# Performance work log

Hardware: AMD Instinct MI355X
Metric: run time of the kernel (lower is better)

## Reference

```python
import jax, jax.numpy as jnp
import numpy as np

N, D, K, A, BINS, DEPTH = 1024, 384, 64, 5, 64, 4
D_MAX = 22.0


def _expected_distance(distogram):
    # distance_one_hot_inverse(softmax(distogram), 0.0, 22.0, 64)
    step = D_MAX / BINS
    centers = step * jnp.arange(BINS, dtype=distogram.dtype) + step / 2
    p = jax.nn.softmax(distogram, axis=-1)  # [N,N,BINS]
    return (p * centers).sum(axis=-1)       # [N,N]


def _extract_neighbours(pos, prev_pos, distogram, resi, chain, batch, mask, key):
    inf = jnp.inf
    same_batch = batch[:, None] == batch[None, :]
    same_chain = (chain[:, None] == chain[None, :]) & same_batch
    pair_mask = mask[:, None] & mask[None, :] & same_batch
    # sequence-separation distance (only within a chain), 3.81 A per residue
    seq_d = jnp.where(same_chain,
                      jnp.abs(resi[:, None] - resi[None, :]).astype(jnp.float32) * 3.81,
                      inf)
    md = _expected_distance(distogram)
    d = jnp.minimum(seq_d, jnp.where(md < 8.0, md, inf))
    ca = pos[:, 1]                                   # current CA positions [N,3]
    d = jnp.minimum(d, jnp.linalg.norm(ca[:, None] - ca[None, :], axis=-1))
    pca = prev_pos[:, 1]
    d = jnp.minimum(d, jnp.linalg.norm(pca[:, None] - pca[None, :], axis=-1))
    d = jnp.where(same_batch, d, inf)
    log_p = -3.0 * d
    u = jax.random.uniform(key, d.shape)
    gumbel = -jnp.log(-jnp.log(u + 1e-6) + 1e-6)
    random_distance = -(log_p + gumbel)
    random_distance = jnp.where(pair_mask, random_distance, inf)
    neg_vals, idx = jax.lax.top_k(-random_distance, K)  # k smallest random distances
    nbr_mask = jnp.isfinite(neg_vals)                   # invalid neighbours have -inf
    return idx, nbr_mask                                # [N,K] int32, [N,K] bool


def setup_inputs() -> dict:
    key = jax.random.key(0)
    ks = jax.random.split(key, 8)
    local = jax.random.normal(ks[0], (N, D), dtype=jnp.float32)
    pos = 3.0 * jax.random.normal(ks[1], (N, A, 3), dtype=jnp.float32)
    prev_pos = 3.0 * jax.random.normal(ks[2], (N, A, 3), dtype=jnp.float32)
    distogram = jax.random.normal(ks[3], (N, N, BINS), dtype=jnp.float32)
    Wn = jax.random.normal(ks[4], (D, D), dtype=jnp.float32) / np.sqrt(D)
    Wp = 0.01 * jax.random.normal(ks[5], (D, A * 3), dtype=jnp.float32)
    ar = jnp.arange(N, dtype=jnp.int32)
    batch = ar // 256          # 4 proteins of 256 residues
    chain = (ar // 128) % 2    # 2 chains per protein
    resi = ar % 128            # residue index within chain
    mask = jnp.ones((N,), dtype=bool)
    return {"local": local, "pos": pos, "prev_pos": prev_pos, "distogram": distogram,
            "Wn": Wn, "Wp": Wp, "resi": resi, "chain": chain, "batch": batch, "mask": mask}


def reference(local, pos, prev_pos, distogram, Wn, Wp, resi, chain, batch, mask):
    mask_f = mask.astype(local.dtype)
    key = jax.random.key(42)
    traj = []
    for t in range(DEPTH):  # diffusion_depth iterations, neighbours recomputed each block
        idx, nbr_mask = _extract_neighbours(pos, prev_pos, distogram, resi, chain,
                                            batch, mask, jax.random.fold_in(key, t))
        nf = local[idx] * nbr_mask[..., None].astype(local.dtype)   # [N,K,D]
        cnt = jnp.maximum(nbr_mask.sum(axis=1, keepdims=True).astype(local.dtype), 1.0)
        msg = nf.sum(axis=1) / cnt                                   # [N,D]
        local = local + jax.nn.gelu(msg @ Wn)
        pos = pos + 0.1 * (local @ Wp).reshape(N, A, 3) * mask_f[:, None, None]
        traj.append(pos)
    trajectory = jnp.stack(traj)  # [DEPTH,N,A,3]
    return local, pos, trajectory
```

## Files before the change

kernel.cpp:

```cpp
#include <hip/hip_runtime.h>
#include <stdint.h>

typedef unsigned int u32;
typedef unsigned long long u64;

#define NN 1024
#define DDIM 384
#define KNB 64
#define BINS_ 64
#define DEPTH_ 4

#define OUT_POS 393216
#define OUT_TRAJ 408576

__device__ __forceinline__ u32 rotl32(u32 x, int r) { return (x << r) | (x >> (32 - r)); }

__device__ __forceinline__ void threefry(u32 k0, u32 k1, u32 x0, u32 x1, u32& o0, u32& o1) {
  u32 ks2 = k0 ^ k1 ^ 0x1BD11BDAu;
#define TF_R(r) { x0 += x1; x1 = rotl32(x1, r); x1 ^= x0; }
  x0 += k0; x1 += k1;
  TF_R(13) TF_R(15) TF_R(26) TF_R(6)
  x0 += k1; x1 += ks2 + 1u;
  TF_R(17) TF_R(29) TF_R(16) TF_R(24)
  x0 += ks2; x1 += k0 + 2u;
  TF_R(13) TF_R(15) TF_R(26) TF_R(6)
  x0 += k0; x1 += k1 + 3u;
  TF_R(17) TF_R(29) TF_R(16) TF_R(24)
  x0 += k1; x1 += ks2 + 4u;
  TF_R(13) TF_R(15) TF_R(26) TF_R(6)
  x0 += ks2; x1 += k0 + 5u;
#undef TF_R
  o0 = x0; o1 = x1;
}

__global__ void k_init(const float* __restrict__ lin, const float* __restrict__ pin,
                       float* __restrict__ localf, float* __restrict__ posf) {
  int id = blockIdx.x * 256 + threadIdx.x;
  if (id < NN * DDIM) localf[id] = lin[id];
  else posf[id - NN * DDIM] = pin[id - NN * DDIM];
}

__global__ __launch_bounds__(256) void k_dstatic(
    const float* __restrict__ disto, const float* __restrict__ ppos,
    const int* __restrict__ resi, const int* __restrict__ chain,
    const int* __restrict__ batch, float* __restrict__ dstat) {
  int p = blockIdx.x * 256 + threadIdx.x;
  int i = p >> 10, j = p & 1023;
  if (batch[i] != batch[j]) { dstat[p] = __builtin_inff(); return; }
  float seq_d = __builtin_inff();
  if (chain[i] == chain[j]) {
    int dr = resi[i] - resi[j];
    seq_d = __fmul_rn(fabsf((float)dr), 3.81f);
  }
  const float4* dp = reinterpret_cast<const float4*>(disto + (size_t)p * BINS_);
  float w[BINS_];
#pragma unroll
  for (int q = 0; q < 16; ++q) {
    float4 v = dp[q];
    w[4*q+0] = v.x; w[4*q+1] = v.y; w[4*q+2] = v.z; w[4*q+3] = v.w;
  }
  float m = -__builtin_inff();
#pragma unroll
  for (int q = 0; q < BINS_; ++q) m = fmaxf(m, w[q]);
  float s = 0.f;
#pragma unroll
  for (int q = 0; q < BINS_; ++q) {
    w[q] = expf(__fsub_rn(w[q], m));
    s = __fadd_rn(s, w[q]);
  }
  float e = 0.f;
#pragma unroll
  for (int q = 0; q < BINS_; ++q) {
    float pq = __fdiv_rn(w[q], s);
    e = __fadd_rn(e, __fmul_rn(pq, 0.34375f * (float)q + 0.171875f));
  }
  float md = e;
  float d = fminf(seq_d, (md < 8.0f) ? md : __builtin_inff());
  float ax = __fsub_rn(ppos[i*15+3], ppos[j*15+3]);
  float ay = __fsub_rn(ppos[i*15+4], ppos[j*15+4]);
  float az = __fsub_rn(ppos[i*15+5], ppos[j*15+5]);
  float ss = __fadd_rn(__fadd_rn(__fmul_rn(ax,ax), __fmul_rn(ay,ay)), __fmul_rn(az,az));
  dstat[p] = fminf(d, __fsqrt_rn(ss));
}

__global__ __launch_bounds__(256) void k_topk(
    const float* __restrict__ dstat, const float* __restrict__ posf,
    const int* __restrict__ batch,
    int t, int* __restrict__ idx, float* __restrict__ cntv) {
  int i = blockIdx.x;
  __shared__ u32 skm[NN];
  __shared__ int sjj[NN];
  int bi = batch[i];
  float cax = posf[i*15+3], cay = posf[i*15+4], caz = posf[i*15+5];
  u32 fk0, fk1;
  threefry(0u, 42u, 0u, (u32)t, fk0, fk1);
  for (int j = threadIdx.x; j < NN; j += 256) {
    float rd = __builtin_inff();
    if (batch[j] == bi) {
      float d = dstat[i*NN + j];
      float dx = __fsub_rn(cax, posf[j*15+3]);
      float dy = __fsub_rn(cay, posf[j*15+4]);
      float dz = __fsub_rn(caz, posf[j*15+5]);
      float ss = __fadd_rn(__fadd_rn(__fmul_rn(dx,dx), __fmul_rn(dy,dy)), __fmul_rn(dz,dz));
      d = fminf(d, __fsqrt_rn(ss));
      u32 o0, o1;
      threefry(fk0, fk1, 0u, (u32)(i*NN + j), o0, o1);
      u32 bits = o0 ^ o1;
      float u = __fsub_rn(__uint_as_float((bits >> 9) | 0x3f800000u), 1.0f);
      float inner = __fadd_rn(-logf(__fadd_rn(u, 1e-6f)), 1e-6f);
      float gum = -logf(inner);
      float logp = __fmul_rn(-3.0f, d);
      rd = -__fadd_rn(logp, gum);
    }
    u32 fb = __float_as_uint(rd);
    u32 km = (fb & 0x80000000u) ? ~fb : (fb | 0x80000000u);
    skm[j] = km; sjj[j] = j;
  }
  for (int size = 2; size <= NN; size <<= 1) {
    for (int stride = size >> 1; stride > 0; stride >>= 1) {
      __syncthreads();
      for (int tt = threadIdx.x; tt < NN/2; tt += 256) {
        int a = ((tt & ~(stride-1)) << 1) | (tt & (stride-1));
        int b = a | stride;
        u32 ka = skm[a], kb = skm[b];
        int ja = sjj[a], jb = sjj[b];
        bool gt = (ka > kb) || ((ka == kb) && (ja > jb));
        bool asc = ((a & size) == 0);
        if (gt == asc) { skm[a] = kb; skm[b] = ka; sjj[a] = jb; sjj[b] = ja; }
      }
    }
  }
  __syncthreads();
  if (threadIdx.x < KNB) {
    u32 km = skm[threadIdx.x];
    bool fin = (km < 0xFF800000u);
    idx[i*KNB + threadIdx.x] = fin ? sjj[threadIdx.x] : -1;
    u64 ball = __ballot(fin);
    if (threadIdx.x == 0) cntv[i] = fmaxf((float)__popcll(ball), 1.0f);
  }
}

__global__ __launch_bounds__(384) void k_msg(
    const float* __restrict__ localf, const int* __restrict__ idx,
    const float* __restrict__ cntv, const float* __restrict__ Wn,
    float* __restrict__ g) {
  int i = blockIdx.x; int d = threadIdx.x;
  __shared__ int sidx[KNB];
  __shared__ float msgL[DDIM];
  if (d < KNB) sidx[d] = idx[i*KNB + d];
  __syncthreads();
  float s = 0.f;
#pragma unroll 8
  for (int k = 0; k < KNB; ++k) {
    int id = sidx[k];
    if (id >= 0) s += localf[id*DDIM + d];
  }
  msgL[d] = s / cntv[i];
  __syncthreads();
  float acc = 0.f;
#pragma unroll 8
  for (int dd = 0; dd < DDIM; ++dd) acc = fmaf(msgL[dd], Wn[dd*DDIM + d], acc);
  float x = acc;
  float th = tanhf(0.7978845608028654f * (x + 0.044715f * x * x * x));
  g[i*DDIM + d] = 0.5f * x * (1.0f + th);
}

__global__ __launch_bounds__(64) void k_update(
    float* __restrict__ localf, const float* __restrict__ g,
    const float* __restrict__ Wp,
    float* __restrict__ posf, float* __restrict__ out, int t) {
  int i = blockIdx.x;
  __shared__ float lr[DDIM];
  for (int d = threadIdx.x; d < DDIM; d += 64) {
    float v = localf[i*DDIM + d] + g[i*DDIM + d];
    localf[i*DDIM + d] = v;
    lr[d] = v;
  }
  __syncthreads();
  if (threadIdx.x < 15) {
    int c = threadIdx.x;
    float acc = 0.f;
#pragma unroll 8
    for (int d = 0; d < DDIM; ++d) acc = fmaf(lr[d], Wp[d*15 + c], acc);
    float pv = posf[i*15 + c] + 0.1f * acc;
    posf[i*15 + c] = pv;
    out[OUT_TRAJ + t*15360 + i*15 + c] = pv;
  }
}

__global__ void k_out(const float* __restrict__ localf, const float* __restrict__ posf,
                      float* __restrict__ out) {
  int id = blockIdx.x * 256 + threadIdx.x;
  if (id < NN * DDIM) out[id] = localf[id];
  else out[id] = posf[id - NN * DDIM];
}

extern "C" void kernel_launch(void* const* d_in, const int* in_sizes, int n_in,
                              void* d_out, int out_size, void* d_ws, size_t ws_size,
                              hipStream_t stream) {
  (void)in_sizes; (void)n_in; (void)out_size; (void)ws_size;
  const float* local_in = (const float*)d_in[0];
  const float* pos_in   = (const float*)d_in[1];
  const float* ppos_in  = (const float*)d_in[2];
  const float* disto    = (const float*)d_in[3];
  const float* Wn       = (const float*)d_in[4];
  const float* Wp       = (const float*)d_in[5];
  const int* resi       = (const int*)d_in[6];
  const int* chain      = (const int*)d_in[7];
  const int* batch      = (const int*)d_in[8];
  float* out = (float*)d_out;
  char* ws = (char*)d_ws;
  float* localf = (float*)(ws + 0);
  float* posf   = (float*)(ws + 1572864);
  float* g      = (float*)(ws + 1634304);
  float* dstat  = (float*)(ws + 3207168);
  int*   idx    = (int*)(ws + 7401472);
  float* cntv   = (float*)(ws + 7663616);

  k_init<<<dim3(1596), dim3(256), 0, stream>>>(local_in, pos_in, localf, posf);
  k_dstatic<<<dim3(4096), dim3(256), 0, stream>>>(disto, ppos_in, resi, chain, batch, dstat);
  for (int t = 0; t < DEPTH_; ++t) {
    k_topk<<<dim3(NN), dim3(256), 0, stream>>>(dstat, posf, batch, t, idx, cntv);
    k_msg<<<dim3(NN), dim3(DDIM), 0, stream>>>(localf, idx, cntv, Wn, g);
    k_update<<<dim3(NN), dim3(64), 0, stream>>>(localf, g, Wp, posf, out, t);
  }
  k_out<<<dim3(1596), dim3(256), 0, stream>>>(localf, posf, out);
}
```

Measured before the change: 661.7 us.

## Fuse top-k, message, and update into one per-round kernel with wave-level sort

Replaces the three per-round kernels with a single k_round kernel that handles four rows per block. Each wave builds 64-bit key/index pairs in registers and selects the top-64 through shuffle-based bitonic sorts and merges, replacing the 1024-element shared-memory bitonic sort with its many __syncthreads. It shares each Wn load across four rows, ping-pongs the local/pos buffers so the init and output copy kernels can go away, and writes the final round straight to the output. The fused kernel launches only 256 blocks, so the GPU may be less fully occupied, and register pressure from the 16 u64 values per lane could cause spills.

```diff
diff --git a/kernel.cpp b/kernel.cpp
--- a/kernel.cpp
+++ b/kernel.cpp
@@ -33,11 +33,23 @@
   o0 = x0; o1 = x1;
 }
 
-__global__ void k_init(const float* __restrict__ lin, const float* __restrict__ pin,
-                       float* __restrict__ localf, float* __restrict__ posf) {
-  int id = blockIdx.x * 256 + threadIdx.x;
-  if (id < NN * DDIM) localf[id] = lin[id];
-  else posf[id - NN * DDIM] = pin[id - NN * DDIM];
+static inline u32 h_rotl32(u32 x, int r) { return (x << r) | (x >> (32 - r)); }
+static void h_threefry(u32 k0, u32 k1, u32 x0, u32 x1, u32& o0, u32& o1) {
+  u32 ks2 = k0 ^ k1 ^ 0x1BD11BDAu;
+#define TF_R(r) { x0 += x1; x1 = h_rotl32(x1, r); x1 ^= x0; }
+  x0 += k0; x1 += k1;
+  TF_R(13) TF_R(15) TF_R(26) TF_R(6)
+  x0 += k1; x1 += ks2 + 1u;
+  TF_R(17) TF_R(29) TF_R(16) TF_R(24)
+  x0 += ks2; x1 += k0 + 2u;
+  TF_R(13) TF_R(15) TF_R(26) TF_R(6)
+  x0 += k0; x1 += k1 + 3u;
+  TF_R(17) TF_R(29) TF_R(16) TF_R(24)
+  x0 += k1; x1 += ks2 + 4u;
+  TF_R(13) TF_R(15) TF_R(26) TF_R(6)
+  x0 += ks2; x1 += k0 + 5u;
+#undef TF_R
+  o0 = x0; o1 = x1;
 }
 
 __global__ __launch_bounds__(256) void k_dstatic(
@@ -83,116 +95,143 @@
   dstat[p] = fminf(d, __fsqrt_rn(ss));
 }
 
-__global__ __launch_bounds__(256) void k_topk(
-    const float* __restrict__ dstat, const float* __restrict__ posf,
-    const int* __restrict__ batch,
-    int t, int* __restrict__ idx, float* __restrict__ cntv) {
-  int i = blockIdx.x;
-  __shared__ u32 skm[NN];
-  __shared__ int sjj[NN];
-  int bi = batch[i];
-  float cax = posf[i*15+3], cay = posf[i*15+4], caz = posf[i*15+5];
-  u32 fk0, fk1;
-  threefry(0u, 42u, 0u, (u32)t, fk0, fk1);
-  for (int j = threadIdx.x; j < NN; j += 256) {
-    float rd = __builtin_inff();
-    if (batch[j] == bi) {
-      float d = dstat[i*NN + j];
-      float dx = __fsub_rn(cax, posf[j*15+3]);
-      float dy = __fsub_rn(cay, posf[j*15+4]);
-      float dz = __fsub_rn(caz, posf[j*15+5]);
-      float ss = __fadd_rn(__fadd_rn(__fmul_rn(dx,dx), __fmul_rn(dy,dy)), __fmul_rn(dz,dz));
-      d = fminf(d, __fsqrt_rn(ss));
-      u32 o0, o1;
-      threefry(fk0, fk1, 0u, (u32)(i*NN + j), o0, o1);
-      u32 bits = o0 ^ o1;
-      float u = __fsub_rn(__uint_as_float((bits >> 9) | 0x3f800000u), 1.0f);
-      float inner = __fadd_rn(-logf(__fadd_rn(u, 1e-6f)), 1e-6f);
-      float gum = -logf(inner);
-      float logp = __fmul_rn(-3.0f, d);
-      rd = -__fadd_rn(logp, gum);
-    }
-    u32 fb = __float_as_uint(rd);
-    u32 km = (fb & 0x80000000u) ? ~fb : (fb | 0x80000000u);
-    skm[j] = km; sjj[j] = j;
-  }
-  for (int size = 2; size <= NN; size <<= 1) {
-    for (int stride = size >> 1; stride > 0; stride >>= 1) {
-      __syncthreads();
-      for (int tt = threadIdx.x; tt < NN/2; tt += 256) {
-        int a = ((tt & ~(stride-1)) << 1) | (tt & (stride-1));
-        int b = a | stride;
-        u32 ka = skm[a], kb = skm[b];
-        int ja = sjj[a], jb = sjj[b];
-        bool gt = (ka > kb) || ((ka == kb) && (ja > jb));
-        bool asc = ((a & size) == 0);
-        if (gt == asc) { skm[a] = kb; skm[b] = ka; sjj[a] = jb; sjj[b] = ja; }
+__device__ __forceinline__ u64 shx64(u64 x, int m) {
+  int lo = __shfl_xor((int)(u32)x, m, 64);
+  int hi = __shfl_xor((int)(u32)(x >> 32), m, 64);
+  return ((u64)(u32)hi << 32) | (u32)lo;
+}
+
+__device__ __forceinline__ u64 merge64(u64 a, u64 b, int lane) {
+  u64 br = shx64(b, 63);
+  u64 m = (a < br) ? a : br;
+  for (int stride = 32; stride > 0; stride >>= 1) {
+    u64 p = shx64(m, stride);
+    u64 lo = (m < p) ? m : p;
+    u64 hi = (m < p) ? p : m;
+    m = ((lane & stride) == 0) ? lo : hi;
+  }
+  return m;
+}
+
+__global__ __launch_bounds__(384) void k_round(
+    const float* __restrict__ dstat, const float* __restrict__ Lprev,
+    float* __restrict__ Lnext, const float* __restrict__ posP,
+    float* __restrict__ posN, const int* __restrict__ batch,
+    const float* __restrict__ Wn, const float* __restrict__ Wp,
+    float* __restrict__ out, int t, u32 fk0, u32 fk1) {
+  __shared__ int sidx[4][KNB];
+  __shared__ float cntL[4];
+  __shared__ float msgT[4][DDIM];
+  __shared__ float lrT[4][DDIM + 1];
+  const int tid = threadIdx.x;
+  const int w = tid >> 6, lane = tid & 63;
+  const int i0 = blockIdx.x * 4;
+
+  if (w < 4) {
+    const int i = i0 + w;
+    const int bi = batch[i];
+    const float cax = posP[i*15+3], cay = posP[i*15+4], caz = posP[i*15+5];
+    u64 v[16];
+#pragma unroll
+    for (int c = 0; c < 16; ++c) {
+      int j = c*64 + lane;
+      float rd = __builtin_inff();
+      if (batch[j] == bi) {
+        float d = dstat[i*NN + j];
+        float dx = __fsub_rn(cax, posP[j*15+3]);
+        float dy = __fsub_rn(cay, posP[j*15+4]);
+        float dz = __fsub_rn(caz, posP[j*15+5]);
+        float ss = __fadd_rn(__fadd_rn(__fmul_rn(dx,dx), __fmul_rn(dy,dy)), __fmul_rn(dz,dz));
+        d = fminf(d, __fsqrt_rn(ss));
+        u32 o0, o1;
+        threefry(fk0, fk1, 0u, (u32)(i*NN + j), o0, o1);
+        u32 bits = o0 ^ o1;
+        float u = __fsub_rn(__uint_as_float((bits >> 9) | 0x3f800000u), 1.0f);
+        float inner = __fadd_rn(-logf(__fadd_rn(u, 1e-6f)), 1e-6f);
+        float gum = -logf(inner);
+        float logp = __fmul_rn(-3.0f, d);
+        rd = -__fadd_rn(logp, gum);
       }
-    }
+      u32 fb = __float_as_uint(rd);
+      u32 km = (fb & 0x80000000u) ? ~fb : (fb | 0x80000000u);
+      v[c] = ((u64)km << 32) | (u32)j;
+    }
+    for (int size = 2; size <= 64; size <<= 1) {
+      for (int stride = size >> 1; stride > 0; stride >>= 1) {
+        bool keepmin = (((lane & stride) == 0) == ((lane & size) == 0));
+#pragma unroll
+        for (int c = 0; c < 16; ++c) {
+          u64 p = shx64(v[c], stride);
+          u64 lo = (v[c] < p) ? v[c] : p;
+          u64 hi = (v[c] < p) ? p : v[c];
+          v[c] = keepmin ? lo : hi;
+        }
+      }
+    }
+#pragma unroll
+    for (int c = 0; c < 8; ++c) v[c] = merge64(v[2*c], v[2*c+1], lane);
+#pragma unroll
+    for (int c = 0; c < 4; ++c) v[c] = merge64(v[2*c], v[2*c+1], lane);
+#pragma unroll
+    for (int c = 0; c < 2; ++c) v[c] = merge64(v[2*c], v[2*c+1], lane);
+    u64 m = merge64(v[0], v[1], lane);
+    u32 km = (u32)(m >> 32);
+    bool fin = (km < 0xFF800000u);
+    sidx[w][lane] = fin ? (int)(u32)(m & 0xffffffffu) : -1;
+    u64 ball = __ballot(fin);
+    if (lane == 0) cntL[w] = fmaxf((float)__popcll(ball), 1.0f);
   }
   __syncthreads();
-  if (threadIdx.x < KNB) {
-    u32 km = skm[threadIdx.x];
-    bool fin = (km < 0xFF800000u);
-    idx[i*KNB + threadIdx.x] = fin ? sjj[threadIdx.x] : -1;
-    u64 ball = __ballot(fin);
-    if (threadIdx.x == 0) cntv[i] = fmaxf((float)__popcll(ball), 1.0f);
-  }
-}
-
-__global__ __launch_bounds__(384) void k_msg(
-    const float* __restrict__ localf, const int* __restrict__ idx,
-    const float* __restrict__ cntv, const float* __restrict__ Wn,
-    float* __restrict__ g) {
-  int i = blockIdx.x; int d = threadIdx.x;
-  __shared__ int sidx[KNB];
-  __shared__ float msgL[DDIM];
-  if (d < KNB) sidx[d] = idx[i*KNB + d];
+
+  {
+    const int c = tid;
+#pragma unroll
+    for (int r = 0; r < 4; ++r) {
+      float s = 0.f;
+#pragma unroll 8
+      for (int k = 0; k < KNB; ++k) {
+        int id = sidx[r][k];
+        if (id >= 0) s += Lprev[id*DDIM + c];
+      }
+      msgT[r][c] = s / cntL[r];
+    }
+  }
   __syncthreads();
-  float s = 0.f;
+
+  {
+    const int c = tid;
+    float a0 = 0.f, a1 = 0.f, a2 = 0.f, a3 = 0.f;
 #pragma unroll 8
-  for (int k = 0; k < KNB; ++k) {
-    int id = sidx[k];
-    if (id >= 0) s += localf[id*DDIM + d];
-  }
-  msgL[d] = s / cntv[i];
+    for (int dd = 0; dd < DDIM; ++dd) {
+      float wv = Wn[dd*DDIM + c];
+      a0 = fmaf(msgT[0][dd], wv, a0);
+      a1 = fmaf(msgT[1][dd], wv, a1);
+      a2 = fmaf(msgT[2][dd], wv, a2);
+      a3 = fmaf(msgT[3][dd], wv, a3);
+    }
+    float accs[4] = {a0, a1, a2, a3};
+#pragma unroll
+    for (int r = 0; r < 4; ++r) {
+      float x = accs[r];
+      float th = tanhf(0.7978845608028654f * (x + 0.044715f * x * x * x));
+      float g = 0.5f * x * (1.0f + th);
+      float ln = Lprev[(i0 + r)*DDIM + c] + g;
+      Lnext[(i0 + r)*DDIM + c] = ln;
+      lrT[r][c] = ln;
+    }
+  }
   __syncthreads();
-  float acc = 0.f;
-#pragma unroll 8
-  for (int dd = 0; dd < DDIM; ++dd) acc = fmaf(msgL[dd], Wn[dd*DDIM + d], acc);
-  float x = acc;
-  float th = tanhf(0.7978845608028654f * (x + 0.044715f * x * x * x));
-  g[i*DDIM + d] = 0.5f * x * (1.0f + th);
-}
-
-__global__ __launch_bounds__(64) void k_update(
-    float* __restrict__ localf, const float* __restrict__ g,
-    const float* __restrict__ Wp,
-    float* __restrict__ posf, float* __restrict__ out, int t) {
-  int i = blockIdx.x;
-  __shared__ float lr[DDIM];
-  for (int d = threadIdx.x; d < DDIM; d += 64) {
-    float v = localf[i*DDIM + d] + g[i*DDIM + d];
-    localf[i*DDIM + d] = v;
-    lr[d] = v;
-  }
-  __syncthreads();
-  if (threadIdx.x < 15) {
-    int c = threadIdx.x;
+
+  if (tid < 60) {
+    const int r = tid / 15, cc = tid % 15;
+    const int i = i0 + r;
     float acc = 0.f;
 #pragma unroll 8
-    for (int d = 0; d < DDIM; ++d) acc = fmaf(lr[d], Wp[d*15 + c], acc);
-    float pv = posf[i*15 + c] + 0.1f * acc;
-    posf[i*15 + c] = pv;
-    out[OUT_TRAJ + t*15360 + i*15 + c] = pv;
-  }
-}
-
-__global__ void k_out(const float* __restrict__ localf, const float* __restrict__ posf,
-                      float* __restrict__ out) {
-  int id = blockIdx.x * 256 + threadIdx.x;
-  if (id < NN * DDIM) out[id] = localf[id];
-  else out[id] = posf[id - NN * DDIM];
+    for (int dd = 0; dd < DDIM; ++dd) acc = fmaf(lrT[r][dd], Wp[dd*15 + cc], acc);
+    float pv = posP[i*15 + cc] + 0.1f * acc;
+    posN[i*15 + cc] = pv;
+    out[OUT_TRAJ + t*15360 + i*15 + cc] = pv;
+  }
 }
 
 extern "C" void kernel_launch(void* const* d_in, const int* in_sizes, int n_in,
@@ -210,19 +249,25 @@
   const int* batch      = (const int*)d_in[8];
   float* out = (float*)d_out;
   char* ws = (char*)d_ws;
-  float* localf = (float*)(ws + 0);
-  float* posf   = (float*)(ws + 1572864);
-  float* g      = (float*)(ws + 1634304);
-  float* dstat  = (float*)(ws + 3207168);
-  int*   idx    = (int*)(ws + 7401472);
-  float* cntv   = (float*)(ws + 7663616);
-
-  k_init<<<dim3(1596), dim3(256), 0, stream>>>(local_in, pos_in, localf, posf);
+  float* dstat = (float*)(ws + 0);
+  float* L0    = (float*)(ws + 4194304);
+  float* L1    = (float*)(ws + 5767168);
+  float* P0    = (float*)(ws + 7340032);
+  float* P1    = (float*)(ws + 7401472);
+
   k_dstatic<<<dim3(4096), dim3(256), 0, stream>>>(disto, ppos_in, resi, chain, batch, dstat);
+
+  const float* Lp = local_in;
+  const float* Pp = pos_in;
+  float* Lbuf[2] = {L0, L1};
+  float* Pbuf[2] = {P0, P1};
   for (int t = 0; t < DEPTH_; ++t) {
-    k_topk<<<dim3(NN), dim3(256), 0, stream>>>(dstat, posf, batch, t, idx, cntv);
-    k_msg<<<dim3(NN), dim3(DDIM), 0, stream>>>(localf, idx, cntv, Wn, g);
-    k_update<<<dim3(NN), dim3(64), 0, stream>>>(localf, g, Wp, posf, out, t);
-  }
-  k_out<<<dim3(1596), dim3(256), 0, stream>>>(localf, posf, out);
-}
+    u32 fk0, fk1;
+    h_threefry(0u, 42u, 0u, (u32)t, fk0, fk1);
+    float* Ln = (t == DEPTH_ - 1) ? out : Lbuf[t & 1];
+    float* Pn = (t == DEPTH_ - 1) ? (out + OUT_POS) : Pbuf[t & 1];
+    k_round<<<dim3(256), dim3(384), 0, stream>>>(dstat, Lp, Ln, Pp, Pn, batch,
+                                                 Wn, Wp, out, t, fk0, fk1);
+    Lp = Ln; Pp = Pn;
+  }
+}
```

After: 687.8 us. 1.04x slower.
